# Kernel optimization log

Hardware: AMD Instinct MI355X
Metric: run time of the kernel (lower is better)

Reference implementation:

```python
import jax, jax.numpy as jnp
import numpy as np

N_CHANNELS = 1024
N_HEADS = 16
BLOCK_SIZE = 2048
BATCH = 4
SEQ = 2048


def setup_inputs() -> dict:
    key = jax.random.key(0)
    k_x, k_wqkv, k_wproj = jax.random.split(key, 3)
    x = jax.random.normal(k_x, (BATCH, SEQ, N_CHANNELS), dtype=jnp.float32)
    # torch nn.Linear: y = x @ W.T + b, W shape [out, in], init normal(std=0.02)
    W_qkv = jax.random.normal(k_wqkv, (3 * N_CHANNELS, N_CHANNELS), dtype=jnp.float32) * 0.02
    b_qkv = jnp.zeros((3 * N_CHANNELS,), dtype=jnp.float32)
    W_proj = jax.random.normal(k_wproj, (N_CHANNELS, N_CHANNELS), dtype=jnp.float32) * 0.02
    b_proj = jnp.zeros((N_CHANNELS,), dtype=jnp.float32)
    return {"x": x, "W_qkv": W_qkv, "b_qkv": b_qkv, "W_proj": W_proj, "b_proj": b_proj}


def reference(x, W_qkv, b_qkv, W_proj, b_proj):
    bs, n, n_channels = x.shape
    n_heads = N_HEADS
    head_dim = n_channels // n_heads
    scale = head_dim ** (-0.5)

    qkv = x @ W_qkv.T + b_qkv                              # [b, n, 3C]
    qkv = qkv.reshape(bs, n, 3, n_heads, head_dim)
    q, k, v = qkv[:, :, 0], qkv[:, :, 1], qkv[:, :, 2]     # [b, n, h, d]

    logits = jnp.einsum('bthc,bshc->bhts', q, k) * scale   # [b, h, t, s]
    # causal mask: log(tril(ones)) = 0 below diagonal, -inf above
    causal = jnp.tril(jnp.ones((n, n), dtype=bool))
    logits = jnp.where(causal[None, None], logits, -jnp.inf)
    attn = jax.nn.softmax(logits, axis=-1)

    output = jnp.einsum('bhts,bshc->bthc', attn, v)        # [b, t, h, d]
    output = output.reshape(bs, n, n_channels)
    output = output @ W_proj.T + b_proj
    return output
```

## Files before the change

kernel.cpp:

```cpp
#include <hip/hip_runtime.h>
#include <hip/hip_bf16.h>
#include <stdint.h>

#define BATCH 4
#define SEQ   2048
#define NC    1024
#define NH    16
#define HD    64
#define NT    16

typedef __bf16 bf16x8 __attribute__((ext_vector_type(8)));
typedef __bf16 bf16x2 __attribute__((ext_vector_type(2)));
typedef float  f32x4  __attribute__((ext_vector_type(4)));
typedef float  f32x16 __attribute__((ext_vector_type(16)));

#define DEV __device__ __forceinline__

DEV unsigned short f2bf(float f) {
    union { float f; unsigned u; } v; v.f = f;
    unsigned r = (v.u + 0x7fffu + ((v.u >> 16) & 1u)) >> 16;
    return (unsigned short)r;
}

DEV float fast_exp2(float x) {
#if __has_builtin(__builtin_amdgcn_exp2f)
    return __builtin_amdgcn_exp2f(x);
#else
    return exp2f(x);
#endif
}

DEV void plane32_swap(uint32_t& a, uint32_t& b) {
#if __has_builtin(__builtin_amdgcn_permlane32_swap)
    auto r = __builtin_amdgcn_permlane32_swap(a, b, false, false);
    a = (uint32_t)r[0];
    b = (uint32_t)r[1];
#else
    uint32_t sa = __shfl_xor(a, 32), sb = __shfl_xor(b, 32);
    const bool hi = ((threadIdx.x & 63) >= 32);
    uint32_t na = hi ? sb : a;
    uint32_t nb = hi ? b : sa;
    a = na; b = nb;
#endif
}

#define GLDS16(gsrc, ldst)                                                           \
    __builtin_amdgcn_global_load_lds(                                                \
        (const __attribute__((address_space(1))) unsigned int*)(gsrc),               \
        (__attribute__((address_space(3))) unsigned int*)(ldst), 16, 0, 0)

#define CVT_N0 (BATCH * SEQ * NC / 4)
#define CVT_N1 (3 * NC * NC / 4)
#define CVT_N2 (NC * NC / 4)

__global__ void cvt_all_kernel(const float* __restrict__ x, unsigned short* __restrict__ xb,
                               const float* __restrict__ wq, unsigned short* __restrict__ wqb,
                               const float* __restrict__ wp, unsigned short* __restrict__ wpb) {
    int i = blockIdx.x * 256 + threadIdx.x;
    const float* src;
    unsigned short* dst;
    if (i < CVT_N0) {
        src = x; dst = xb;
    } else if (i < CVT_N0 + CVT_N1) {
        i -= CVT_N0; src = wq; dst = wqb;
    } else {
        i -= CVT_N0 + CVT_N1; src = wp; dst = wpb;
    }
    float4 v = reinterpret_cast<const float4*>(src)[i];
    ushort4 o;
    o.x = f2bf(v.x); o.y = f2bf(v.y); o.z = f2bf(v.z); o.w = f2bf(v.w);
    reinterpret_cast<ushort4*>(dst)[i] = o;
}

template <bool BF16_OUT>
__global__ __launch_bounds__(256, 2) void gemm_bt_kernel(
    const unsigned short* __restrict__ A,
    const unsigned short* __restrict__ W,
    const float* __restrict__ bias,
    void* __restrict__ Cout,
    int M, int N, int K, int scale_n, float scale)
{
    __shared__ __align__(16) char Alds[128 * 128];
    __shared__ __align__(16) char Blds[128 * 128];

    const int tid = threadIdx.x;
    const int w = tid >> 6, l = tid & 63, g = l >> 4, lr = l & 15;
    const int nt = N >> 7;
    const int cpx = gridDim.x >> 3;
    const int bid = (blockIdx.x & 7) * cpx + (blockIdx.x >> 3);
    const int mtile = bid / nt, ntile = bid % nt;
    const int m0 = mtile << 7, n0 = ntile << 7;
    const int wr = (w >> 1) << 6, wc = (w & 1) << 6;

    f32x4 acc[4][4] = {};

    for (int kt = 0; kt < K; kt += 64) {
        if (kt) __syncthreads();
#pragma unroll
        for (int i = 0; i < 4; ++i) {
            const int issue = (i << 2) + w;
            const int row = (issue << 3) + (l >> 3);
            const int chunk = (l & 7) ^ (row & 7);
            GLDS16((const char*)(A + (size_t)(m0 + row) * K + kt) + (chunk << 4),
                   Alds + (issue << 10));
        }
#pragma unroll
        for (int i = 0; i < 4; ++i) {
            const int issue = (i << 2) + w;
            const int row = (issue << 3) + (l >> 3);
            const int chunk = (l & 7) ^ (row & 7);
            GLDS16((const char*)(W + (size_t)(n0 + row) * K + kt) + (chunk << 4),
                   Blds + (issue << 10));
        }
        __syncthreads();

#pragma unroll
        for (int kb = 0; kb < 2; ++kb) {
            bf16x8 af[4], bfr[4];
#pragma unroll
            for (int mf = 0; mf < 4; ++mf) {
                const int row = wr + (mf << 4) + lr;
                const int chunk = ((kb << 2) + g) ^ (row & 7);
                af[mf] = *reinterpret_cast<const bf16x8*>(Alds + row * 128 + (chunk << 4));
            }
#pragma unroll
            for (int nf = 0; nf < 4; ++nf) {
                const int row = wc + (nf << 4) + lr;
                const int chunk = ((kb << 2) + g) ^ (row & 7);
                bfr[nf] = *reinterpret_cast<const bf16x8*>(Blds + row * 128 + (chunk << 4));
            }
#pragma unroll
            for (int mf = 0; mf < 4; ++mf)
#pragma unroll
                for (int nf = 0; nf < 4; ++nf)
                    acc[mf][nf] = __builtin_amdgcn_mfma_f32_16x16x32_bf16(
                        af[mf], bfr[nf], acc[mf][nf], 0, 0, 0);
        }
    }

#pragma unroll
    for (int mf = 0; mf < 4; ++mf) {
#pragma unroll
        for (int nf = 0; nf < 4; ++nf) {
            const int n = n0 + wc + (nf << 4) + lr;
            const float bscale = (n < scale_n) ? scale : 1.0f;
            const float bv = bias[n];
#pragma unroll
            for (int r = 0; r < 4; ++r) {
                const int m = m0 + wr + (mf << 4) + (g << 2) + r;
                float v2 = (acc[mf][nf][r] + bv) * bscale;
                if (BF16_OUT)
                    ((unsigned short*)Cout)[(size_t)m * N + n] = f2bf(v2);
                else
                    ((float*)Cout)[(size_t)m * N + n] = v2;
            }
        }
    }
}

__global__ __launch_bounds__(256, 2) void gemm_bt64_kernel(
    const unsigned short* __restrict__ A,
    const unsigned short* __restrict__ W,
    const float* __restrict__ bias,
    float* __restrict__ Cout,
    int M, int N, int K)
{
    __shared__ __align__(16) char Alds[64 * 128];
    __shared__ __align__(16) char Blds[128 * 128];

    const int tid = threadIdx.x;
    const int w = tid >> 6, l = tid & 63, g = l >> 4, lr = l & 15;
    const int nt = N >> 7;
    const int cpx = gridDim.x >> 3;
    const int bid = (blockIdx.x & 7) * cpx + (blockIdx.x >> 3);
    const int mtile = bid / nt, ntile = bid % nt;
    const int m0 = mtile << 6, n0 = ntile << 7;
    const int wr = (w >> 1) << 5, wc = (w & 1) << 6;

    f32x4 acc[2][4] = {};

    for (int kt = 0; kt < K; kt += 64) {
        if (kt) __syncthreads();
#pragma unroll
        for (int i = 0; i < 2; ++i) {
            const int issue = (i << 2) + w;
            const int row = (issue << 3) + (l >> 3);
            const int chunk = (l & 7) ^ (row & 7);
            GLDS16((const char*)(A + (size_t)(m0 + row) * K + kt) + (chunk << 4),
                   Alds + (issue << 10));
        }
#pragma unroll
        for (int i = 0; i < 4; ++i) {
            const int issue = (i << 2) + w;
            const int row = (issue << 3) + (l >> 3);
            const int chunk = (l & 7) ^ (row & 7);
            GLDS16((const char*)(W + (size_t)(n0 + row) * K + kt) + (chunk << 4),
                   Blds + (issue << 10));
        }
        __syncthreads();

#pragma unroll
        for (int kb = 0; kb < 2; ++kb) {
            bf16x8 af[2], bfr[4];
#pragma unroll
            for (int mf = 0; mf < 2; ++mf) {
                const int row = wr + (mf << 4) + lr;
                const int chunk = ((kb << 2) + g) ^ (row & 7);
                af[mf] = *reinterpret_cast<const bf16x8*>(Alds + row * 128 + (chunk << 4));
            }
#pragma unroll
            for (int nf = 0; nf < 4; ++nf) {
                const int row = wc + (nf << 4) + lr;
                const int chunk = ((kb << 2) + g) ^ (row & 7);
                bfr[nf] = *reinterpret_cast<const bf16x8*>(Blds + row * 128 + (chunk << 4));
            }
#pragma unroll
            for (int mf = 0; mf < 2; ++mf)
#pragma unroll
                for (int nf = 0; nf < 4; ++nf)
                    acc[mf][nf] = __builtin_amdgcn_mfma_f32_16x16x32_bf16(
                        af[mf], bfr[nf], acc[mf][nf], 0, 0, 0);
        }
    }

#pragma unroll
    for (int mf = 0; mf < 2; ++mf) {
#pragma unroll
        for (int nf = 0; nf < 4; ++nf) {
            const int n = n0 + wc + (nf << 4) + lr;
            const float bv = bias[n];
#pragma unroll
            for (int r = 0; r < 4; ++r) {
                const int m = m0 + wr + (mf << 4) + (g << 2) + r;
                Cout[(size_t)m * N + n] = acc[mf][nf][r] + bv;
            }
        }
    }
}

__global__ __launch_bounds__(256, 4) void attn_kernel(
    const unsigned short* __restrict__ qkv,
    unsigned short* __restrict__ ctx)
{
    __shared__ __align__(16) char Klds[2][8192];
    __shared__ __align__(16) char Vt[2][64 * 144];

    const int tid = threadIdx.x;
    const int w = tid >> 6, l = tid & 63, hi = l >> 5, lq = l & 31;
    const int bid = blockIdx.x;
    const int qt = NT - 1 - (bid >> 6);
    const int h = (bid >> 2) & 15, b = bid & 3;
    const unsigned short* base = qkv + (size_t)b * SEQ * 3072 + h * 64;

    const int vkey0 = (tid >> 5) << 3;
    const int vd0   = (tid & 31) << 1;
    const unsigned short* vbase = base + 2048 + (size_t)vkey0 * 3072 + vd0;

    const int q0 = (qt << 7) + (w << 5);
    const int q = q0 + lq;
    const int ntiles = (qt + 1) << 1;

    bf16x8 qfr[4];
#pragma unroll
    for (int ds = 0; ds < 4; ++ds)
        qfr[ds] = *reinterpret_cast<const bf16x8*>(
            base + (size_t)q * 3072 + (ds << 4) + (hi << 3));

    f32x16 acc0 = {}, acc1 = {};
    float lrun = 0.f;

    uint32_t vreg[8];

#pragma unroll
    for (int i = 0; i < 8; ++i)
        vreg[i] = *reinterpret_cast<const uint32_t*>(vbase + (size_t)i * 3072);
#pragma unroll
    for (int i = 0; i < 2; ++i) {
        const int issue = (i << 2) + w;
        const int row = (issue << 3) + (l >> 3);
        const int chunk = (l & 7) ^ (row & 7);
        GLDS16((const char*)(base + 1024 + (size_t)row * 3072) + (chunk << 4),
               Klds[0] + (issue << 10));
    }
    {
        uint4 a, bq;
        a.x = (vreg[0] & 0xffffu) | (vreg[1] << 16);
        a.y = (vreg[2] & 0xffffu) | (vreg[3] << 16);
        a.z = (vreg[4] & 0xffffu) | (vreg[5] << 16);
        a.w = (vreg[6] & 0xffffu) | (vreg[7] << 16);
        bq.x = (vreg[0] >> 16) | (vreg[1] & 0xffff0000u);
        bq.y = (vreg[2] >> 16) | (vreg[3] & 0xffff0000u);
        bq.z = (vreg[4] >> 16) | (vreg[5] & 0xffff0000u);
        bq.w = (vreg[6] >> 16) | (vreg[7] & 0xffff0000u);
        *reinterpret_cast<uint4*>(Vt[0] + vd0 * 144 + vkey0 * 2) = a;
        *reinterpret_cast<uint4*>(Vt[0] + (vd0 + 1) * 144 + vkey0 * 2) = bq;
    }
    __syncthreads();

    for (int t = 0; t < ntiles; ++t) {
        const int cur = t & 1;
        const int kv0 = t << 6;
        const bool pf_ = (t + 1 < ntiles);

        if (pf_) {
            const int kv1 = kv0 + 64;
#pragma unroll
            for (int i = 0; i < 8; ++i)
                vreg[i] = *reinterpret_cast<const uint32_t*>(
                    vbase + (size_t)(kv1 + i) * 3072);
#pragma unroll
            for (int i = 0; i < 2; ++i) {
                const int issue = (i << 2) + w;
                const int row = (issue << 3) + (l >> 3);
                const int chunk = (l & 7) ^ (row & 7);
                GLDS16((const char*)(base + 1024 + (size_t)(kv1 + row) * 3072) + (chunk << 4),
                       Klds[cur ^ 1] + (issue << 10));
            }
        }

        if (kv0 <= q0 + 31) {
            const bool do1 = (kv0 + 32 <= q0 + 31);

            f32x16 st0 = {}, st1 = {};
#pragma unroll
            for (int ds = 0; ds < 4; ++ds) {
                const int chunk = (((ds << 1) + hi) ^ (lq & 7)) << 4;
                bf16x8 k0 = *reinterpret_cast<const bf16x8*>(
                    Klds[cur] + lq * 128 + chunk);
                st0 = __builtin_amdgcn_mfma_f32_32x32x16_bf16(k0, qfr[ds], st0, 0, 0, 0);
            }
            if (do1) {
#pragma unroll
                for (int ds = 0; ds < 4; ++ds) {
                    const int chunk = (((ds << 1) + hi) ^ (lq & 7)) << 4;
                    bf16x8 k1 = *reinterpret_cast<const bf16x8*>(
                        Klds[cur] + (lq + 32) * 128 + chunk);
                    st1 = __builtin_amdgcn_mfma_f32_32x32x16_bf16(k1, qfr[ds], st1, 0, 0, 0);
                }
            }

            if (kv0 + 31 > q0) {
#pragma unroll
                for (int r = 0; r < 16; ++r) {
                    const int key = kv0 + ((r & 3) + ((r >> 2) << 3) + (hi << 2));
                    if (key > q) st0[r] = -INFINITY;
                }
            }
            if (do1 && kv0 + 63 > q0) {
#pragma unroll
                for (int r = 0; r < 16; ++r) {
                    const int key = kv0 + 32 + ((r & 3) + ((r >> 2) << 3) + (hi << 2));
                    if (key > q) st1[r] = -INFINITY;
                }
            }

            float rs = 0.f;
#pragma unroll
            for (int r = 0; r < 16; ++r) { st0[r] = fast_exp2(st0[r]); rs += st0[r]; }
            if (do1) {
#pragma unroll
                for (int r = 0; r < 16; ++r) { st1[r] = fast_exp2(st1[r]); rs += st1[r]; }
            }
            lrun += rs;

            uint32_t pk0[8], pk1[8];
#pragma unroll
            for (int sp = 0; sp < 4; ++sp)
#pragma unroll
                for (int c = 0; c < 2; ++c) {
                    bf16x2 t0 = {(__bf16)st0[(sp << 2) + (c << 1)],
                                 (__bf16)st0[(sp << 2) + (c << 1) + 1]};
                    pk0[(sp << 1) + c] = __builtin_bit_cast(uint32_t, t0);
                }
            if (do1) {
#pragma unroll
                for (int sp = 0; sp < 4; ++sp)
#pragma unroll
                    for (int c = 0; c < 2; ++c) {
                        bf16x2 t1 = {(__bf16)st1[(sp << 2) + (c << 1)],
                                     (__bf16)st1[(sp << 2) + (c << 1) + 1]};
                        pk1[(sp << 1) + c] = __builtin_bit_cast(uint32_t, t1);
                    }
            }

            const int nkt = do1 ? 4 : 2;
#pragma unroll
            for (int kt = 0; kt < 4; ++kt) {
                if (kt >= nkt) break;
                const int s0 = (kt & 1) << 1;
                uint32_t x0, x1, y0, y1;
                if (kt < 2) {
                    x0 = pk0[(s0 << 1) + 0]; x1 = pk0[(s0 << 1) + 1];
                    y0 = pk0[(s0 << 1) + 2]; y1 = pk0[(s0 << 1) + 3];
                } else {
                    x0 = pk1[(s0 << 1) + 0]; x1 = pk1[(s0 << 1) + 1];
                    y0 = pk1[(s0 << 1) + 2]; y1 = pk1[(s0 << 1) + 3];
                }
                plane32_swap(x0, y0);
                plane32_swap(x1, y1);
                union { uint32_t u[4]; bf16x8 v; } pf;
                pf.u[0] = x0; pf.u[1] = x1; pf.u[2] = y0; pf.u[3] = y1;

                const char* vrow = Vt[cur] + ((kt << 4) + (hi << 3)) * 2;
                bf16x8 vf0 = *reinterpret_cast<const bf16x8*>(vrow + lq * 144);
                bf16x8 vf1 = *reinterpret_cast<const bf16x8*>(vrow + (lq + 32) * 144);
                acc0 = __builtin_amdgcn_mfma_f32_32x32x16_bf16(vf0, pf.v, acc0, 0, 0, 0);
                acc1 = __builtin_amdgcn_mfma_f32_32x32x16_bf16(vf1, pf.v, acc1, 0, 0, 0);
            }
        }

        if (pf_) {
            uint4 a, bq;
            a.x = (vreg[0] & 0xffffu) | (vreg[1] << 16);
            a.y = (vreg[2] & 0xffffu) | (vreg[3] << 16);
            a.z = (vreg[4] & 0xffffu) | (vreg[5] << 16);
            a.w = (vreg[6] & 0xffffu) | (vreg[7] << 16);
            bq.x = (vreg[0] >> 16) | (vreg[1] & 0xffff0000u);
            bq.y = (vreg[2] >> 16) | (vreg[3] & 0xffff0000u);
            bq.z = (vreg[4] >> 16) | (vreg[5] & 0xffff0000u);
            bq.w = (vreg[6] >> 16) | (vreg[7] & 0xffff0000u);
            char* vt = Vt[cur ^ 1];
            *reinterpret_cast<uint4*>(vt + vd0 * 144 + vkey0 * 2) = a;
            *reinterpret_cast<uint4*>(vt + (vd0 + 1) * 144 + vkey0 * 2) = bq;
            __syncthreads();
        }
    }

    {
        const float ltot = lrun + __shfl_xor(lrun, 32);
        const float li = 1.0f / ltot;
        unsigned short* op = ctx + (size_t)(b * SEQ + q) * NC + h * HD;
#pragma unroll
        for (int r = 0; r < 16; ++r) {
            const int d = (r & 3) + ((r >> 2) << 3) + (hi << 2);
            op[d] = f2bf(acc0[r] * li);
            op[d + 32] = f2bf(acc1[r] * li);
        }
    }
}

extern "C" void kernel_launch(void* const* d_in, const int* in_sizes, int n_in,
                              void* d_out, int out_size, void* d_ws, size_t ws_size,
                              hipStream_t stream) {
    const float* x     = (const float*)d_in[0];
    const float* Wqkv  = (const float*)d_in[1];
    const float* bqkv  = (const float*)d_in[2];
    const float* Wproj = (const float*)d_in[3];
    const float* bproj = (const float*)d_in[4];
    float* out = (float*)d_out;

    const int M = BATCH * SEQ;
    unsigned short* ws = (unsigned short*)d_ws;
    unsigned short* xb     = ws;
    unsigned short* wqkvb  = xb + (size_t)M * NC;
    unsigned short* wprojb = wqkvb + (size_t)3 * NC * NC;
    unsigned short* qkvb   = wprojb + (size_t)NC * NC;
    unsigned short* ctxb   = qkvb + (size_t)M * 3 * NC;

    {
        const int total = CVT_N0 + CVT_N1 + CVT_N2;
        cvt_all_kernel<<<(total + 255) / 256, 256, 0, stream>>>(
            x, xb, Wqkv, wqkvb, Wproj, wprojb);
    }

    gemm_bt_kernel<true><<<(M / 128) * (3 * NC / 128), 256, 0, stream>>>(
        xb, wqkvb, bqkv, qkvb, M, 3 * NC, NC, NC, 0.18033688011112042f);

    attn_kernel<<<NT * NH * BATCH, 256, 0, stream>>>(qkvb, ctxb);

    gemm_bt64_kernel<<<(M / 64) * (NC / 128), 256, 0, stream>>>(
        ctxb, wprojb, bproj, out, M, NC, NC);
}
```

Baseline: 150.5 us.

## Software-pipeline attention PV MFMA one tile behind QK with triple-buffered V

Restructures the attention loop so that the P·V MFMAs of the previous tile are issued right after the QK MFMAs of the current tile. This lets the softmax exp and pack work overlap with matrix-core work instead of serialising them. V tiles move to a three-deep LDS ring with an XOR-swizzled 128-byte row layout in place of the padded 144-byte stride, and the MFMA section runs under raised wave priority via s_setprio. The cost is extra LDS, live pk registers carried across iterations, and a tail PV after the loop, which may reduce occupancy.

Result: slower. 189.7 us (+26.1%).

```diff
diff --git a/kernel.cpp b/kernel.cpp
--- a/kernel.cpp
+++ b/kernel.cpp
@@ -243,7 +243,7 @@
     unsigned short* __restrict__ ctx)
 {
     __shared__ __align__(16) char Klds[2][8192];
-    __shared__ __align__(16) char Vt[2][64 * 144];
+    __shared__ __align__(16) char Vt[3][8192];
 
     const int tid = threadIdx.x;
     const int w = tid >> 6, l = tid & 63, hi = l >> 5, lq = l & 31;
@@ -254,6 +254,9 @@
 
     const int vkey0 = (tid >> 5) << 3;
     const int vd0   = (tid & 31) << 1;
+    const int vcc0  = tid >> 5;
+    const int vph1  = (vcc0 ^ (vd0 & 7)) << 4;
+    const int vph2  = (vcc0 ^ ((vd0 + 1) & 7)) << 4;
     const unsigned short* vbase = base + 2048 + (size_t)vkey0 * 3072 + vd0;
 
     const int q0 = (qt << 7) + (w << 5);
@@ -268,8 +271,41 @@
 
     f32x16 acc0 = {}, acc1 = {};
     float lrun = 0.f;
-
     uint32_t vreg[8];
+    uint32_t pk0[8], pk1[8];
+    bool havePrev = false, prevDo1 = false;
+    int prevV = 0;
+
+    auto doPV = [&](int vbuf, bool pdo1) {
+        const int nkt = pdo1 ? 4 : 2;
+        const int fch = lq & 7;
+        const char* Vl = Vt[vbuf];
+#pragma unroll
+        for (int kt = 0; kt < 4; ++kt) {
+            if (kt >= nkt) break;
+            const int s0 = (kt & 1) << 1;
+            uint32_t x0, x1, y0, y1;
+            if (kt < 2) {
+                x0 = pk0[(s0 << 1) + 0]; x1 = pk0[(s0 << 1) + 1];
+                y0 = pk0[(s0 << 1) + 2]; y1 = pk0[(s0 << 1) + 3];
+            } else {
+                x0 = pk1[(s0 << 1) + 0]; x1 = pk1[(s0 << 1) + 1];
+                y0 = pk1[(s0 << 1) + 2]; y1 = pk1[(s0 << 1) + 3];
+            }
+            plane32_swap(x0, y0);
+            plane32_swap(x1, y1);
+            union { uint32_t u[4]; bf16x8 v; } pf;
+            pf.u[0] = x0; pf.u[1] = x1; pf.u[2] = y0; pf.u[3] = y1;
+
+            const int cc = (kt << 1) + hi;
+            bf16x8 vf0 = *reinterpret_cast<const bf16x8*>(
+                Vl + lq * 128 + ((cc ^ fch) << 4));
+            bf16x8 vf1 = *reinterpret_cast<const bf16x8*>(
+                Vl + (lq + 32) * 128 + ((cc ^ fch) << 4));
+            acc0 = __builtin_amdgcn_mfma_f32_32x32x16_bf16(vf0, pf.v, acc0, 0, 0, 0);
+            acc1 = __builtin_amdgcn_mfma_f32_32x32x16_bf16(vf1, pf.v, acc1, 0, 0, 0);
+        }
+    };
 
 #pragma unroll
     for (int i = 0; i < 8; ++i)
@@ -292,13 +328,13 @@
         bq.y = (vreg[2] >> 16) | (vreg[3] & 0xffff0000u);
         bq.z = (vreg[4] >> 16) | (vreg[5] & 0xffff0000u);
         bq.w = (vreg[6] >> 16) | (vreg[7] & 0xffff0000u);
-        *reinterpret_cast<uint4*>(Vt[0] + vd0 * 144 + vkey0 * 2) = a;
-        *reinterpret_cast<uint4*>(Vt[0] + (vd0 + 1) * 144 + vkey0 * 2) = bq;
+        *reinterpret_cast<uint4*>(Vt[0] + vd0 * 128 + vph1) = a;
+        *reinterpret_cast<uint4*>(Vt[0] + (vd0 + 1) * 128 + vph2) = bq;
     }
     __syncthreads();
 
     for (int t = 0; t < ntiles; ++t) {
-        const int cur = t & 1;
+        const int kcur = t & 1;
         const int kv0 = t << 6;
         const bool pf_ = (t + 1 < ntiles);
 
@@ -314,19 +350,22 @@
                 const int row = (issue << 3) + (l >> 3);
                 const int chunk = (l & 7) ^ (row & 7);
                 GLDS16((const char*)(base + 1024 + (size_t)(kv1 + row) * 3072) + (chunk << 4),
-                       Klds[cur ^ 1] + (issue << 10));
-            }
-        }
-
-        if (kv0 <= q0 + 31) {
-            const bool do1 = (kv0 + 32 <= q0 + 31);
-
-            f32x16 st0 = {}, st1 = {};
+                       Klds[kcur ^ 1] + (issue << 10));
+            }
+        }
+
+        const bool doQK = (kv0 <= q0 + 31);
+        const bool do1  = (kv0 + 32 <= q0 + 31);
+        const bool firePV = havePrev;
+        f32x16 st0 = {}, st1 = {};
+
+        __builtin_amdgcn_s_setprio(1);
+        if (doQK) {
 #pragma unroll
             for (int ds = 0; ds < 4; ++ds) {
                 const int chunk = (((ds << 1) + hi) ^ (lq & 7)) << 4;
                 bf16x8 k0 = *reinterpret_cast<const bf16x8*>(
-                    Klds[cur] + lq * 128 + chunk);
+                    Klds[kcur] + lq * 128 + chunk);
                 st0 = __builtin_amdgcn_mfma_f32_32x32x16_bf16(k0, qfr[ds], st0, 0, 0, 0);
             }
             if (do1) {
@@ -334,11 +373,16 @@
                 for (int ds = 0; ds < 4; ++ds) {
                     const int chunk = (((ds << 1) + hi) ^ (lq & 7)) << 4;
                     bf16x8 k1 = *reinterpret_cast<const bf16x8*>(
-                        Klds[cur] + (lq + 32) * 128 + chunk);
+                        Klds[kcur] + (lq + 32) * 128 + chunk);
                     st1 = __builtin_amdgcn_mfma_f32_32x32x16_bf16(k1, qfr[ds], st1, 0, 0, 0);
                 }
             }
-
+        }
+        if (firePV) doPV(prevV, prevDo1);
+        __builtin_amdgcn_s_setprio(0);
+        havePrev = false;
+
+        if (doQK) {
             if (kv0 + 31 > q0) {
 #pragma unroll
                 for (int r = 0; r < 16; ++r) {
@@ -363,7 +407,6 @@
             }
             lrun += rs;
 
-            uint32_t pk0[8], pk1[8];
 #pragma unroll
             for (int sp = 0; sp < 4; ++sp)
 #pragma unroll
@@ -382,31 +425,7 @@
                         pk1[(sp << 1) + c] = __builtin_bit_cast(uint32_t, t1);
                     }
             }
-
-            const int nkt = do1 ? 4 : 2;
-#pragma unroll
-            for (int kt = 0; kt < 4; ++kt) {
-                if (kt >= nkt) break;
-                const int s0 = (kt & 1) << 1;
-                uint32_t x0, x1, y0, y1;
-                if (kt < 2) {
-                    x0 = pk0[(s0 << 1) + 0]; x1 = pk0[(s0 << 1) + 1];
-                    y0 = pk0[(s0 << 1) + 2]; y1 = pk0[(s0 << 1) + 3];
-                } else {
-                    x0 = pk1[(s0 << 1) + 0]; x1 = pk1[(s0 << 1) + 1];
-                    y0 = pk1[(s0 << 1) + 2]; y1 = pk1[(s0 << 1) + 3];
-                }
-                plane32_swap(x0, y0);
-                plane32_swap(x1, y1);
-                union { uint32_t u[4]; bf16x8 v; } pf;
-                pf.u[0] = x0; pf.u[1] = x1; pf.u[2] = y0; pf.u[3] = y1;
-
-                const char* vrow = Vt[cur] + ((kt << 4) + (hi << 3)) * 2;
-                bf16x8 vf0 = *reinterpret_cast<const bf16x8*>(vrow + lq * 144);
-                bf16x8 vf1 = *reinterpret_cast<const bf16x8*>(vrow + (lq + 32) * 144);
-                acc0 = __builtin_amdgcn_mfma_f32_32x32x16_bf16(vf0, pf.v, acc0, 0, 0, 0);
-                acc1 = __builtin_amdgcn_mfma_f32_32x32x16_bf16(vf1, pf.v, acc1, 0, 0, 0);
-            }
+            havePrev = true; prevDo1 = do1; prevV = t % 3;
         }
 
         if (pf_) {
@@ -419,12 +438,14 @@
             bq.y = (vreg[2] >> 16) | (vreg[3] & 0xffff0000u);
             bq.z = (vreg[4] >> 16) | (vreg[5] & 0xffff0000u);
             bq.w = (vreg[6] >> 16) | (vreg[7] & 0xffff0000u);
-            char* vt = Vt[cur ^ 1];
-            *reinterpret_cast<uint4*>(vt + vd0 * 144 + vkey0 * 2) = a;
-            *reinterpret_cast<uint4*>(vt + (vd0 + 1) * 144 + vkey0 * 2) = bq;
+            char* vt = Vt[(t + 1) % 3];
+            *reinterpret_cast<uint4*>(vt + vd0 * 128 + vph1) = a;
+            *reinterpret_cast<uint4*>(vt + (vd0 + 1) * 128 + vph2) = bq;
             __syncthreads();
         }
     }
+
+    if (havePrev) doPV(prevV, prevDo1);
 
     {
         const float ltot = lrun + __shfl_xor(lrun, 32);
```
